# Optimization experiments

Measured on AMD Instinct MI355X. Metric: run time of the kernel, lower is better.

## Reference

```python
import jax, jax.numpy as jnp
import numpy as np

K = 8          # opt.pk, explicit precision cutoff
MARGIN = 0.2   # opt.margin
NEG = -1e30    # sentinel for masked sort keys


def setup_inputs() -> dict:
    key = jax.random.key(0)
    k1, k2 = jax.random.split(key)
    batch_reprs = jax.random.normal(k1, (4096, 512), dtype=jnp.float32)
    batch_labels = jax.random.randint(k2, (4096,), 0, 64)
    return {"batch_reprs": batch_reprs, "batch_labels": batch_labels}


def _forward(batch_reprs, batch_labels):
    B = batch_reprs.shape[0]
    dt = batch_reprs.dtype
    # cls_match_mat: 1 if same class
    match = (batch_labels[:, None] == batch_labels[None, :]).astype(dt)
    # pairwise euclidean distance (squared=False), safe sqrt at zero diagonal
    sq = jnp.sum(batch_reprs * batch_reprs, axis=1)
    res = jnp.maximum(sq[:, None] - 2.0 * (batch_reprs @ batch_reprs.T) + sq[None, :], 0.0)
    zero = res <= 0.0
    d = jnp.where(zero, 0.0, jnp.sqrt(jnp.where(zero, 1.0, res)))
    sim_hat = -d + (1.0 - match) * MARGIN  # use_margin=True path
    # rank via double argsort (descending similarity -> rank 1 = best)
    order = jnp.argsort(-sim_hat, axis=1)
    rank = jnp.argsort(order, axis=1).astype(dt) + 1.0
    pos_nums = jnp.sum(match, axis=1)
    ks = jnp.minimum(pos_nums, jnp.asarray(K + 1, dt))[:, None]  # k_mat per row
    w = 1.0 / jnp.log2(rank + 1.0) + 1.0  # DCG-style rank weight
    # false positives: not same class, within top-k_i
    fp_mask = (match < 1.0) & (rank <= ks)
    fp_nums = jnp.sum(fp_mask, axis=1)  # |N| per row
    # false negatives: same class, beyond top-k_i
    fn_mask = (match > 0.0) & (rank > ks)
    fp_term = jnp.sum(jnp.where(fp_mask, sim_hat * w, 0.0))
    # per-row variable-size topk over false negatives, vectorized:
    # mask non-FN entries to -inf, sort desc, keep first fp_nums[i] entries
    fn_key = jnp.where(fn_mask, sim_hat, NEG)
    fn_order = jnp.argsort(-fn_key, axis=1)
    sorted_sim = jnp.take_along_axis(sim_hat, fn_order, axis=1)
    sorted_w = jnp.take_along_axis(w, fn_order, axis=1)
    sorted_valid = jnp.take_along_axis(fn_mask, fn_order, axis=1)
    take = (jnp.arange(B)[None, :].astype(dt) < fp_nums[:, None]) & sorted_valid
    fn_term = jnp.sum(jnp.where(take, sorted_sim * sorted_w, 0.0))
    # rows with fp_num==0 contribute 0 to both terms, matching the host loop
    return fp_term - fn_term


def reference(batch_reprs, batch_labels):
    return _forward(batch_reprs, batch_labels)
```

## Files before the change

kernel.cpp:

```cpp
#include <hip/hip_runtime.h>
#include <math.h>

#define BB 4096
#define DD 512
#define KTOP 9
#define MARGIN_F 0.2f
#define NT 32
#define NTRI (NT * (NT + 1) / 2)

typedef __attribute__((ext_vector_type(8))) short short8;
typedef __attribute__((ext_vector_type(4))) float f32x4;
typedef unsigned long long u64;

__device__ unsigned short g_Rhi[(size_t)BB * DD];
__device__ u64 g_cmask[64 * 64];

__device__ __forceinline__ unsigned short f2bf(float x) {
  unsigned u = __float_as_uint(x);
  u += 0x7fffu + ((u >> 16) & 1u);
  return (unsigned short)(u >> 16);
}

__device__ __forceinline__ float ord16val(unsigned o16) {
  unsigned e = (o16 << 16) | 0x8000u;
  unsigned s = (e & 0x80000000u) ? (e ^ 0x80000000u) : ~e;
  return __uint_as_float(s);
}

__device__ __forceinline__ unsigned wavemax32_dpp(unsigned c) {
#define MSTEP(CTRL, RM)                                                        \
  {                                                                            \
    unsigned o = (unsigned)__builtin_amdgcn_update_dpp(0, (int)c, CTRL, RM, 0xf, false); \
    if (o > c) c = o;                                                          \
  }
  MSTEP(0xB1, 0xf) MSTEP(0x4E, 0xf) MSTEP(0x141, 0xf) MSTEP(0x140, 0xf)
  MSTEP(0x142, 0xa) MSTEP(0x143, 0xc)
#undef MSTEP
  return (unsigned)__builtin_amdgcn_readlane((int)c, 63);
}

__device__ __forceinline__ int wavesum_dpp(int c) {
#define SSTEP(CTRL, RM)                                                        \
  c += __builtin_amdgcn_update_dpp(0, c, CTRL, RM, 0xf, false);
  SSTEP(0xB1, 0xf) SSTEP(0x4E, 0xf) SSTEP(0x141, 0xf) SSTEP(0x140, 0xf)
  SSTEP(0x142, 0xa) SSTEP(0x143, 0xc)
#undef SSTEP
  return __builtin_amdgcn_readlane(c, 63);
}

__device__ __forceinline__ unsigned u4c(const uint4& f, int q) {
  return q == 0 ? f.x : q == 1 ? f.y : q == 2 ? f.z : f.w;
}

__global__ __launch_bounds__(64) void splitsq(const float* __restrict__ R,
                                              float* __restrict__ sq) {
  const int row = blockIdx.x, lane = threadIdx.x;
  const float4* r4 = (const float4*)(R + (size_t)row * DD);
  float4 a = r4[lane], b = r4[lane + 64];
  float xs[8] = {a.x, a.y, a.z, a.w, b.x, b.y, b.z, b.w};
  unsigned short hs[8];
  float s = 0.f;
  #pragma unroll
  for (int q = 0; q < 8; ++q) {
    float x = xs[q];
    s += x * x;
    hs[q] = f2bf(x);
  }
  const size_t base = (size_t)row * DD;
  *(ushort4*)&g_Rhi[base + lane * 4]       = *(ushort4*)&hs[0];
  *(ushort4*)&g_Rhi[base + 256 + lane * 4] = *(ushort4*)&hs[4];
  #pragma unroll
  for (int off = 32; off; off >>= 1) s += __shfl_down(s, off);
  if (lane == 0) sq[row] = s;
}

__global__ __launch_bounds__(64) void buildmask(const int* __restrict__ labels) {
  __shared__ int slab[BB];
  const int c = blockIdx.x, lane = threadIdx.x;
  for (int i = lane; i < BB / 4; i += 64) ((int4*)slab)[i] = ((const int4*)labels)[i];
  __syncthreads();
  u64 m = 0;
  #pragma unroll
  for (int e = 0; e < 64; ++e) {
    int j = 512 * (e >> 3) + 8 * lane + (e & 7);
    m |= (u64)(slab[j] == c) << e;
  }
  g_cmask[c * 64 + lane] = m;
}

__global__ __launch_bounds__(256, 2) void simgemm_rs2(const int* __restrict__ labels,
                                                      const float* __restrict__ sq,
                                                      unsigned short* __restrict__ simq) {
  const int x = blockIdx.x & 7;
  int c = blockIdx.x >> 3;
  int bi = 0, bj = 0;
  #pragma unroll
  for (int q = 0; q < 4; ++q) {
    const int bjq = (q < 2) ? (2 * x + q) : (28 - 2 * x + q);
    const int n = bjq + 1;
    if (c >= 0 && c < n) { bj = bjq; bi = c; }
    c -= n;
  }
  const int i0 = bi * 128, j0 = bj * 128;

  __shared__ __align__(16) unsigned char smembytes[65536];
  unsigned short (*kbuf)[2][8192] = (unsigned short (*)[2][8192])smembytes;

  const int tid = threadIdx.x;
  const int wid = tid >> 6, lane = tid & 63;
  const int wr = wid >> 1, wc = wid & 1;
  const int lrow = lane & 15, kblk = lane >> 4;

  const int sr = lane & 15;
  const int sc = (lane >> 4) * 8;
  const int r0 = (2 * wid + 0) * 16 + sr;
  const int r1 = (2 * wid + 1) * 16 + sr;
  const unsigned short* gA0 = &g_Rhi[(size_t)(i0 + r0) * DD + sc];
  const unsigned short* gA1 = &g_Rhi[(size_t)(i0 + r1) * DD + sc];
  const unsigned short* gB0 = &g_Rhi[(size_t)(j0 + r0) * DD + sc];
  const unsigned short* gB1 = &g_Rhi[(size_t)(j0 + r1) * DD + sc];

  f32x4 acc[4][4] = {};
  uint4 vA00, vA01, vA10, vA11, vB00, vB01, vB10, vB11;

#define STAGE_LOAD(K0)                                                         \
  vA00 = *(const uint4*)(gA0 + (K0));      vB00 = *(const uint4*)(gB0 + (K0)); \
  vA01 = *(const uint4*)(gA0 + (K0) + 32); vB01 = *(const uint4*)(gB0 + (K0) + 32); \
  vA10 = *(const uint4*)(gA1 + (K0));      vB10 = *(const uint4*)(gB1 + (K0)); \
  vA11 = *(const uint4*)(gA1 + (K0) + 32); vB11 = *(const uint4*)(gB1 + (K0) + 32);

#define STAGE_WRITE(BUF)                                                       \
  {                                                                            \
    const int c0 = (2 * wid + 0) * 1024 + lane * 8;                            \
    const int c1 = (2 * wid + 1) * 1024 + lane * 8;                            \
    *(uint4*)&kbuf[BUF][0][c0]       = vA00; *(uint4*)&kbuf[BUF][1][c0]       = vB00; \
    *(uint4*)&kbuf[BUF][0][c0 + 512] = vA01; *(uint4*)&kbuf[BUF][1][c0 + 512] = vB01; \
    *(uint4*)&kbuf[BUF][0][c1]       = vA10; *(uint4*)&kbuf[BUF][1][c1]       = vB10; \
    *(uint4*)&kbuf[BUF][0][c1 + 512] = vA11; *(uint4*)&kbuf[BUF][1][c1 + 512] = vB11; \
  }

  STAGE_LOAD(0);
  STAGE_WRITE(0);
  STAGE_LOAD(64);
  __syncthreads();

  for (int step = 0; step < 8; ++step) {
    const int cur = step & 1;

    #pragma unroll
    for (int kk = 0; kk < 2; ++kk) {
      short8 a[4], b[4];
      #pragma unroll
      for (int m = 0; m < 4; ++m)
        a[m] = *(const short8*)&kbuf[cur][0][(wr * 4 + m) * 1024 + kk * 512 + lane * 8];
      #pragma unroll
      for (int n = 0; n < 4; ++n)
        b[n] = *(const short8*)&kbuf[cur][1][(wc * 4 + n) * 1024 + kk * 512 + lane * 8];
      #pragma unroll
      for (int m = 0; m < 4; ++m) {
        #pragma unroll
        for (int n = 0; n < 4; ++n) {
          acc[m][n] = __builtin_amdgcn_mfma_f32_16x16x32_bf16(a[m], b[n], acc[m][n], 0, 0, 0);
        }
      }
    }

    if (step < 7) {
      STAGE_WRITE(cur ^ 1);
      if (step < 6) { STAGE_LOAD((step + 2) * 64); }
      __syncthreads();
    }
  }
#undef STAGE_LOAD
#undef STAGE_WRITE

  __syncthreads();
  unsigned short (*T)[132] = (unsigned short (*)[132])smembytes;
  float* sqi = (float*)(smembytes + 33792);
  float* sqj = (float*)(smembytes + 34304);
  int* labi  = (int*)(smembytes + 34816);
  int* labj  = (int*)(smembytes + 35328);
  if (tid < 128) { sqi[tid] = sq[i0 + tid]; labi[tid] = labels[i0 + tid]; }
  else { int t2 = tid - 128; sqj[t2] = sq[j0 + t2]; labj[t2] = labels[j0 + t2]; }
  __syncthreads();

  #pragma unroll
  for (int m = 0; m < 4; ++m) {
    const int rbase = wr * 64 + m * 16 + kblk * 4;
    #pragma unroll
    for (int n = 0; n < 4; ++n) {
      const int ccol = wc * 64 + n * 16 + lrow;
      const float sqc = sqj[ccol];
      const int lc_ = labj[ccol];
      #pragma unroll
      for (int reg = 0; reg < 4; ++reg) {
        const int r = rbase + reg;
        float res = sqi[r] - 2.0f * acc[m][n][reg] + sqc;
        float dd = (res <= 0.f) ? 0.f : sqrtf(res);
        float sv = -dd + ((labi[r] != lc_) ? MARGIN_F : 0.f);
        unsigned su = __float_as_uint(sv);
        unsigned ord = su ^ ((unsigned)((int)su >> 31) | 0x80000000u);
        T[r][ccol] = (unsigned short)(ord >> 16);
      }
    }
  }
  __syncthreads();

  const int srow0 = tid >> 4, scol0 = (tid & 15) * 8;
  #pragma unroll
  for (int p = 0; p < 8; ++p) {
    const int r = p * 16 + srow0;
    short8 w = *(const short8*)&T[r][scol0];
    *(short8*)&simq[(size_t)(i0 + r) * BB + j0 + scol0] = w;
  }
  if (bi != bj) {
    #pragma unroll
    for (int p = 0; p < 8; ++p) {
      const int col = p * 16 + srow0;
      unsigned short tmp[8];
      #pragma unroll
      for (int t = 0; t < 8; ++t) tmp[t] = T[scol0 + t][col];
      *(short8*)&simq[(size_t)(j0 + col) * BB + i0 + scol0] = *(short8*)tmp;
    }
  }
}

#define TOP2UPD(k, a, b) {                                                     \
  unsigned _mx = ((k) > (a)) ? (k) : (a);                                      \
  unsigned _mn = ((k) > (a)) ? (a) : (k);                                      \
  (a) = _mx;                                                                   \
  (b) = (_mn > (b)) ? _mn : (b); }

__global__ __launch_bounds__(256) void rowproc7(const unsigned short* __restrict__ simq,
                                                const int* __restrict__ labels,
                                                float* __restrict__ partials) {
  const int tid = threadIdx.x;
  const int lane = tid & 63;
  const int row = blockIdx.x * 4 + (tid >> 6);

  const int myl = labels[row];
  const u64 mask = g_cmask[myl * 64 + lane];
  const unsigned lbase2 = (unsigned)((4095 - 8 * lane) << 1);

  const uint4* rowp = (const uint4*)(simq + (size_t)row * BB);
  unsigned k[64];
  #pragma unroll
  for (int s = 0; s < 8; ++s) {
    uint4 w = rowp[lane + s * 64];
    const unsigned base_s = lbase2 - (unsigned)(1024 * s);
    #pragma unroll
    for (int q = 0; q < 4; ++q) {
      const unsigned wv = u4c(w, q);
      const int e0 = s * 8 + q * 2;
      k[e0]     = ((wv & 0xffffu) << 13)
                | (base_s - (unsigned)((q * 2) << 1)     + (unsigned)((mask >> e0) & 1ull));
      k[e0 + 1] = ((wv >> 16) << 13)
                | (base_s - (unsigned)((q * 2 + 1) << 1) + (unsigned)((mask >> (e0 + 1)) & 1ull));
    }
  }

  unsigned h1 = 0, h2 = 0;
  #pragma unroll
  for (int e = 0; e < 64; ++e) TOP2UPD(k[e], h1, h2);
  const int pos = wavesum_dpp(__popcll(mask));
  const int ks = min(pos, KTOP);

  unsigned kth = 0;
  float fp = 0.f; int fpn = 0;
  #pragma unroll
  for (int t = 0; t < KTOP; ++t) {
    if (t < ks) {
      unsigned g = wavemax32_dpp(h1);
      if (!(g & 1u)) { fp += ord16val(g >> 13) * (1.f / log2f((float)(t + 2)) + 1.f); fpn++; }
      if (t == ks - 1) kth = g;
      if (h1 == g) {
        h1 = h2; h2 = ~0u;
        if (h1 == ~0u) {
          h1 = 0; h2 = 0;
          #pragma unroll
          for (int e = 0; e < 64; ++e) {
            if (k[e] < g) TOP2UPD(k[e], h1, h2);
          }
        }
      }
    }
  }

  float fn = 0.f;
  if (fpn > 0) {
    unsigned f1 = 0, f2 = 0;
    #pragma unroll
    for (int e = 0; e < 64; ++e) {
      if ((k[e] & 1u) && k[e] < kth) TOP2UPD(k[e], f1, f2);
    }
    unsigned ck[KTOP];
    int nc = 0;
    #pragma unroll
    for (int u = 0; u < KTOP; ++u) {
      ck[u] = ~0u;
      if (u < fpn) {
        unsigned g = wavemax32_dpp(f1);
        if (g != 0u) {
          ck[u] = g; nc = u + 1;
          if (f1 == g) {
            f1 = f2; f2 = ~0u;
            if (f1 == ~0u) {
              f1 = 0; f2 = 0;
              #pragma unroll
              for (int e = 0; e < 64; ++e) {
                if ((k[e] & 1u) && k[e] < g) TOP2UPD(k[e], f1, f2);
              }
            }
          }
        }
      }
    }
    if (nc > 0) {
      int cnt[KTOP];
      #pragma unroll
      for (int u = 0; u < KTOP; ++u) cnt[u] = 0;
      #pragma unroll
      for (int e = 0; e < 64; ++e) {
        #pragma unroll
        for (int u = 0; u < KTOP; ++u) cnt[u] += (k[e] > ck[u]) ? 1 : 0;
      }
      #pragma unroll
      for (int u = 0; u < KTOP; ++u) cnt[u] = wavesum_dpp(cnt[u]);
      #pragma unroll
      for (int u = 0; u < KTOP; ++u) {
        if (u < nc) {
          int rank = 1 + cnt[u];
          fn += ord16val(ck[u] >> 13) * (1.f / log2f((float)(rank + 1)) + 1.f);
        }
      }
    }
  }

  if (lane == 0) partials[row] = fp - fn;
}

__global__ __launch_bounds__(256) void finalreduce(const float* __restrict__ partials,
                                                   float* __restrict__ out) {
  __shared__ float s[256];
  const int tid = threadIdx.x;
  float acc = 0.f;
  for (int j = tid; j < BB; j += 256) acc += partials[j];
  s[tid] = acc; __syncthreads();
  #pragma unroll
  for (int st = 128; st; st >>= 1) { if (tid < st) s[tid] += s[tid + st]; __syncthreads(); }
  if (tid == 0) out[0] = s[0];
}

extern "C" void kernel_launch(void* const* d_in, const int* in_sizes, int n_in,
                              void* d_out, int out_size, void* d_ws, size_t ws_size,
                              hipStream_t stream) {
  const float* R      = (const float*)d_in[0];
  const int*   labels = (const int*)d_in[1];
  float* out = (float*)d_out;

  unsigned short* simq = (unsigned short*)d_ws;
  float* sq            = (float*)((char*)d_ws + (size_t)BB * BB * 2);
  float* partials      = sq + BB;

  splitsq<<<BB, 64, 0, stream>>>(R, sq);
  buildmask<<<64, 64, 0, stream>>>(labels);
  simgemm_rs2<<<NTRI, 256, 0, stream>>>(labels, sq, simq);
  rowproc7<<<BB / 4, 256, 0, stream>>>(simq, labels, partials);
  finalreduce<<<1, 256, 0, stream>>>(partials, out);
}
```

Before: 93.88 us.

## Process four rows per wave in rowproc with software-prefetched next-row loads

Each wave in the row-processing kernel now handles four consecutive rows instead of one. It prefetches the next row's packed similarity data and class mask into registers while running the top-k selection on the current row. The grid shrinks from 1024 to 256 blocks, with launch bounds set to one block per SM. This aims to hide global-load latency behind the DPP reductions, at the cost of higher register pressure and fewer waves to hide latency across the GPU.

```diff
diff --git a/kernel.cpp b/kernel.cpp
--- a/kernel.cpp
+++ b/kernel.cpp
@@ -46,10 +46,6 @@
   SSTEP(0x142, 0xa) SSTEP(0x143, 0xc)
 #undef SSTEP
   return __builtin_amdgcn_readlane(c, 63);
-}
-
-__device__ __forceinline__ unsigned u4c(const uint4& f, int q) {
-  return q == 0 ? f.x : q == 1 ? f.y : q == 2 ? f.z : f.w;
 }
 
 __global__ __launch_bounds__(64) void splitsq(const float* __restrict__ R,
@@ -231,112 +227,135 @@
   (a) = _mx;                                                                   \
   (b) = (_mn > (b)) ? _mn : (b); }
 
-__global__ __launch_bounds__(256) void rowproc7(const unsigned short* __restrict__ simq,
-                                                const int* __restrict__ labels,
-                                                float* __restrict__ partials) {
+#define KB(S, W)                                                               \
+  {                                                                            \
+    const unsigned base_s = lbase2 - (unsigned)(1024 * (S));                   \
+    k[(S)*8+0] = (((W).x & 0xffffu) << 13) | (base_s -  0u + (unsigned)((mask >> ((S)*8+0)) & 1ull)); \
+    k[(S)*8+1] = (((W).x >> 16)     << 13) | (base_s -  2u + (unsigned)((mask >> ((S)*8+1)) & 1ull)); \
+    k[(S)*8+2] = (((W).y & 0xffffu) << 13) | (base_s -  4u + (unsigned)((mask >> ((S)*8+2)) & 1ull)); \
+    k[(S)*8+3] = (((W).y >> 16)     << 13) | (base_s -  6u + (unsigned)((mask >> ((S)*8+3)) & 1ull)); \
+    k[(S)*8+4] = (((W).z & 0xffffu) << 13) | (base_s -  8u + (unsigned)((mask >> ((S)*8+4)) & 1ull)); \
+    k[(S)*8+5] = (((W).z >> 16)     << 13) | (base_s - 10u + (unsigned)((mask >> ((S)*8+5)) & 1ull)); \
+    k[(S)*8+6] = (((W).w & 0xffffu) << 13) | (base_s - 12u + (unsigned)((mask >> ((S)*8+6)) & 1ull)); \
+    k[(S)*8+7] = (((W).w >> 16)     << 13) | (base_s - 14u + (unsigned)((mask >> ((S)*8+7)) & 1ull)); \
+  }
+
+__global__ __launch_bounds__(256, 1) void rowproc8(const unsigned short* __restrict__ simq,
+                                                   const int* __restrict__ labels,
+                                                   float* __restrict__ partials) {
   const int tid = threadIdx.x;
   const int lane = tid & 63;
-  const int row = blockIdx.x * 4 + (tid >> 6);
-
-  const int myl = labels[row];
-  const u64 mask = g_cmask[myl * 64 + lane];
+  const int row0 = blockIdx.x * 16 + (tid >> 6) * 4;
   const unsigned lbase2 = (unsigned)((4095 - 8 * lane) << 1);
 
-  const uint4* rowp = (const uint4*)(simq + (size_t)row * BB);
-  unsigned k[64];
-  #pragma unroll
-  for (int s = 0; s < 8; ++s) {
-    uint4 w = rowp[lane + s * 64];
-    const unsigned base_s = lbase2 - (unsigned)(1024 * s);
-    #pragma unroll
-    for (int q = 0; q < 4; ++q) {
-      const unsigned wv = u4c(w, q);
-      const int e0 = s * 8 + q * 2;
-      k[e0]     = ((wv & 0xffffu) << 13)
-                | (base_s - (unsigned)((q * 2) << 1)     + (unsigned)((mask >> e0) & 1ull));
-      k[e0 + 1] = ((wv >> 16) << 13)
-                | (base_s - (unsigned)((q * 2 + 1) << 1) + (unsigned)((mask >> (e0 + 1)) & 1ull));
-    }
-  }
-
-  unsigned h1 = 0, h2 = 0;
-  #pragma unroll
-  for (int e = 0; e < 64; ++e) TOP2UPD(k[e], h1, h2);
-  const int pos = wavesum_dpp(__popcll(mask));
-  const int ks = min(pos, KTOP);
-
-  unsigned kth = 0;
-  float fp = 0.f; int fpn = 0;
-  #pragma unroll
-  for (int t = 0; t < KTOP; ++t) {
-    if (t < ks) {
-      unsigned g = wavemax32_dpp(h1);
-      if (!(g & 1u)) { fp += ord16val(g >> 13) * (1.f / log2f((float)(t + 2)) + 1.f); fpn++; }
-      if (t == ks - 1) kth = g;
-      if (h1 == g) {
-        h1 = h2; h2 = ~0u;
-        if (h1 == ~0u) {
-          h1 = 0; h2 = 0;
-          #pragma unroll
-          for (int e = 0; e < 64; ++e) {
-            if (k[e] < g) TOP2UPD(k[e], h1, h2);
+  uint4 w0, w1, w2, w3, w4, w5, w6, w7;
+  {
+    const uint4* rp = (const uint4*)(simq + (size_t)row0 * BB);
+    w0 = rp[lane];       w1 = rp[lane + 64];  w2 = rp[lane + 128]; w3 = rp[lane + 192];
+    w4 = rp[lane + 256]; w5 = rp[lane + 320]; w6 = rp[lane + 384]; w7 = rp[lane + 448];
+  }
+  int myl = labels[row0];
+  u64 mask = g_cmask[myl * 64 + lane];
+
+  for (int rr = 0; rr < 4; ++rr) {
+    const int row = row0 + rr;
+
+    unsigned k[64];
+    KB(0, w0) KB(1, w1) KB(2, w2) KB(3, w3)
+    KB(4, w4) KB(5, w5) KB(6, w6) KB(7, w7)
+    const int pos = wavesum_dpp(__popcll(mask));
+    const int ks = min(pos, KTOP);
+
+    int nlab = 0;
+    if (rr < 3) {
+      const uint4* rp = (const uint4*)(simq + (size_t)(row + 1) * BB);
+      w0 = rp[lane];       w1 = rp[lane + 64];  w2 = rp[lane + 128]; w3 = rp[lane + 192];
+      w4 = rp[lane + 256]; w5 = rp[lane + 320]; w6 = rp[lane + 384]; w7 = rp[lane + 448];
+      nlab = labels[row + 1];
+    }
+
+    unsigned h1 = 0, h2 = 0;
+    #pragma unroll
+    for (int e = 0; e < 64; ++e) TOP2UPD(k[e], h1, h2);
+
+    unsigned kth = 0;
+    float fp = 0.f; int fpn = 0;
+    #pragma unroll
+    for (int t = 0; t < KTOP; ++t) {
+      if (t < ks) {
+        unsigned g = wavemax32_dpp(h1);
+        if (!(g & 1u)) { fp += ord16val(g >> 13) * (1.f / log2f((float)(t + 2)) + 1.f); fpn++; }
+        if (t == ks - 1) kth = g;
+        if (h1 == g) {
+          h1 = h2; h2 = ~0u;
+          if (h1 == ~0u) {
+            h1 = 0; h2 = 0;
+            #pragma unroll
+            for (int e = 0; e < 64; ++e) {
+              if (k[e] < g) TOP2UPD(k[e], h1, h2);
+            }
           }
         }
       }
     }
-  }
-
-  float fn = 0.f;
-  if (fpn > 0) {
-    unsigned f1 = 0, f2 = 0;
-    #pragma unroll
-    for (int e = 0; e < 64; ++e) {
-      if ((k[e] & 1u) && k[e] < kth) TOP2UPD(k[e], f1, f2);
-    }
-    unsigned ck[KTOP];
-    int nc = 0;
-    #pragma unroll
-    for (int u = 0; u < KTOP; ++u) {
-      ck[u] = ~0u;
-      if (u < fpn) {
-        unsigned g = wavemax32_dpp(f1);
-        if (g != 0u) {
-          ck[u] = g; nc = u + 1;
-          if (f1 == g) {
-            f1 = f2; f2 = ~0u;
-            if (f1 == ~0u) {
-              f1 = 0; f2 = 0;
-              #pragma unroll
-              for (int e = 0; e < 64; ++e) {
-                if ((k[e] & 1u) && k[e] < g) TOP2UPD(k[e], f1, f2);
+
+    u64 nmask = 0;
+    if (rr < 3) nmask = g_cmask[nlab * 64 + lane];
+
+    float fn = 0.f;
+    if (fpn > 0) {
+      unsigned f1 = 0, f2 = 0;
+      #pragma unroll
+      for (int e = 0; e < 64; ++e) {
+        if ((k[e] & 1u) && k[e] < kth) TOP2UPD(k[e], f1, f2);
+      }
+      unsigned ck[KTOP];
+      int nc = 0;
+      #pragma unroll
+      for (int u = 0; u < KTOP; ++u) {
+        ck[u] = ~0u;
+        if (u < fpn) {
+          unsigned g = wavemax32_dpp(f1);
+          if (g != 0u) {
+            ck[u] = g; nc = u + 1;
+            if (f1 == g) {
+              f1 = f2; f2 = ~0u;
+              if (f1 == ~0u) {
+                f1 = 0; f2 = 0;
+                #pragma unroll
+                for (int e = 0; e < 64; ++e) {
+                  if ((k[e] & 1u) && k[e] < g) TOP2UPD(k[e], f1, f2);
+                }
               }
             }
           }
         }
       }
-    }
-    if (nc > 0) {
-      int cnt[KTOP];
-      #pragma unroll
-      for (int u = 0; u < KTOP; ++u) cnt[u] = 0;
-      #pragma unroll
-      for (int e = 0; e < 64; ++e) {
-        #pragma unroll
-        for (int u = 0; u < KTOP; ++u) cnt[u] += (k[e] > ck[u]) ? 1 : 0;
-      }
-      #pragma unroll
-      for (int u = 0; u < KTOP; ++u) cnt[u] = wavesum_dpp(cnt[u]);
-      #pragma unroll
-      for (int u = 0; u < KTOP; ++u) {
-        if (u < nc) {
-          int rank = 1 + cnt[u];
-          fn += ord16val(ck[u] >> 13) * (1.f / log2f((float)(rank + 1)) + 1.f);
-        }
-      }
-    }
-  }
-
-  if (lane == 0) partials[row] = fp - fn;
+      if (nc > 0) {
+        int cnt[KTOP];
+        #pragma unroll
+        for (int u = 0; u < KTOP; ++u) cnt[u] = 0;
+        #pragma unroll
+        for (int e = 0; e < 64; ++e) {
+          #pragma unroll
+          for (int u = 0; u < KTOP; ++u) cnt[u] += (k[e] > ck[u]) ? 1 : 0;
+        }
+        #pragma unroll
+        for (int u = 0; u < KTOP; ++u) cnt[u] = wavesum_dpp(cnt[u]);
+        #pragma unroll
+        for (int u = 0; u < KTOP; ++u) {
+          if (u < nc) {
+            int rank = 1 + cnt[u];
+            fn += ord16val(ck[u] >> 13) * (1.f / log2f((float)(rank + 1)) + 1.f);
+          }
+        }
+      }
+    }
+
+    if (lane == 0) partials[row] = fp - fn;
+    myl = nlab;
+    mask = nmask;
+  }
 }
 
 __global__ __launch_bounds__(256) void finalreduce(const float* __restrict__ partials,
@@ -365,6 +384,6 @@
   splitsq<<<BB, 64, 0, stream>>>(R, sq);
   buildmask<<<64, 64, 0, stream>>>(labels);
   simgemm_rs2<<<NTRI, 256, 0, stream>>>(labels, sq, simq);
-  rowproc7<<<BB / 4, 256, 0, stream>>>(simq, labels, partials);
+  rowproc8<<<256, 256, 0, stream>>>(simq, labels, partials);
   finalreduce<<<1, 256, 0, stream>>>(partials, out);
 }
```

After: 118.0 us. +25.7%, slower.

## Split each row's top-k selection across two waves with shared-memory merges

Applied to the files above, without the earlier changes.

Row processing now runs one row per 128-thread block, and each of its two wavefronts holds half of the row's 4096 keys (32 per lane instead of 64). Wave-level max and count results are merged through shared memory with block barriers. The aim is to halve per-lane register pressure and serial scan length, raising occupancy and latency hiding. The cost is extra __syncthreads per selection step and twice as many waves per row.

```diff
diff --git a/kernel.cpp b/kernel.cpp
--- a/kernel.cpp
+++ b/kernel.cpp
@@ -231,46 +231,65 @@
   (a) = _mx;                                                                   \
   (b) = (_mn > (b)) ? _mn : (b); }
 
-__global__ __launch_bounds__(256) void rowproc7(const unsigned short* __restrict__ simq,
+__global__ __launch_bounds__(128) void rowproc9(const unsigned short* __restrict__ simq,
                                                 const int* __restrict__ labels,
                                                 float* __restrict__ partials) {
+  __shared__ unsigned sred[2 * KTOP + 2][2];
+  __shared__ int sint[2 + 2 * KTOP];
+
   const int tid = threadIdx.x;
   const int lane = tid & 63;
-  const int row = blockIdx.x * 4 + (tid >> 6);
+  const int h = tid >> 6;
+  const int row = blockIdx.x;
+
+  const uint4* rp = (const uint4*)(simq + (size_t)row * BB);
+  uint4 w0 = rp[lane + (4 * h + 0) * 64];
+  uint4 w1 = rp[lane + (4 * h + 1) * 64];
+  uint4 w2 = rp[lane + (4 * h + 2) * 64];
+  uint4 w3 = rp[lane + (4 * h + 3) * 64];
 
   const int myl = labels[row];
-  const u64 mask = g_cmask[myl * 64 + lane];
+  const unsigned mh = (unsigned)(g_cmask[myl * 64 + lane] >> (32 * h));
   const unsigned lbase2 = (unsigned)((4095 - 8 * lane) << 1);
 
-  const uint4* rowp = (const uint4*)(simq + (size_t)row * BB);
-  unsigned k[64];
-  #pragma unroll
-  for (int s = 0; s < 8; ++s) {
-    uint4 w = rowp[lane + s * 64];
-    const unsigned base_s = lbase2 - (unsigned)(1024 * s);
+  unsigned k[32];
+  #pragma unroll
+  for (int s = 0; s < 4; ++s) {
+    const uint4 w = s == 0 ? w0 : s == 1 ? w1 : s == 2 ? w2 : w3;
+    const unsigned base_s = lbase2 - (unsigned)(1024 * (4 * h + s));
     #pragma unroll
     for (int q = 0; q < 4; ++q) {
       const unsigned wv = u4c(w, q);
       const int e0 = s * 8 + q * 2;
       k[e0]     = ((wv & 0xffffu) << 13)
-                | (base_s - (unsigned)((q * 2) << 1)     + (unsigned)((mask >> e0) & 1ull));
+                | (base_s - (unsigned)((q * 2) << 1)     + ((mh >> e0) & 1u));
       k[e0 + 1] = ((wv >> 16) << 13)
-                | (base_s - (unsigned)((q * 2 + 1) << 1) + (unsigned)((mask >> (e0 + 1)) & 1ull));
-    }
-  }
+                | (base_s - (unsigned)((q * 2 + 1) << 1) + ((mh >> (e0 + 1)) & 1u));
+    }
+  }
+
+  {
+    int p = wavesum_dpp(__popc(mh));
+    sint[h] = p;
+  }
+  __syncthreads();
+  const int pos = sint[0] + sint[1];
+  const int ks = min(pos, KTOP);
 
   unsigned h1 = 0, h2 = 0;
   #pragma unroll
-  for (int e = 0; e < 64; ++e) TOP2UPD(k[e], h1, h2);
-  const int pos = wavesum_dpp(__popcll(mask));
-  const int ks = min(pos, KTOP);
+  for (int e = 0; e < 32; ++e) TOP2UPD(k[e], h1, h2);
 
   unsigned kth = 0;
   float fp = 0.f; int fpn = 0;
   #pragma unroll
   for (int t = 0; t < KTOP; ++t) {
     if (t < ks) {
-      unsigned g = wavemax32_dpp(h1);
+      sred[t][h] = wavemax32_dpp(h1);
+    }
+    __syncthreads();
+    if (t < ks) {
+      const unsigned g = max(sred[t][0], sred[t][1]);
       if (!(g & 1u)) { fp += ord16val(g >> 13) * (1.f / log2f((float)(t + 2)) + 1.f); fpn++; }
       if (t == ks - 1) kth = g;
       if (h1 == g) {
@@ -278,7 +297,7 @@
         if (h1 == ~0u) {
           h1 = 0; h2 = 0;
           #pragma unroll
-          for (int e = 0; e < 64; ++e) {
+          for (int e = 0; e < 32; ++e) {
             if (k[e] < g) TOP2UPD(k[e], h1, h2);
           }
         }
@@ -290,7 +309,7 @@
   if (fpn > 0) {
     unsigned f1 = 0, f2 = 0;
     #pragma unroll
-    for (int e = 0; e < 64; ++e) {
+    for (int e = 0; e < 32; ++e) {
       if ((k[e] & 1u) && k[e] < kth) TOP2UPD(k[e], f1, f2);
     }
     unsigned ck[KTOP];
@@ -299,7 +318,11 @@
     for (int u = 0; u < KTOP; ++u) {
       ck[u] = ~0u;
       if (u < fpn) {
-        unsigned g = wavemax32_dpp(f1);
+        sred[KTOP + 1 + u][h] = wavemax32_dpp(f1);
+      }
+      __syncthreads();
+      if (u < fpn) {
+        const unsigned g = max(sred[KTOP + 1 + u][0], sred[KTOP + 1 + u][1]);
         if (g != 0u) {
           ck[u] = g; nc = u + 1;
           if (f1 == g) {
@@ -307,7 +330,7 @@
             if (f1 == ~0u) {
               f1 = 0; f2 = 0;
               #pragma unroll
-              for (int e = 0; e < 64; ++e) {
+              for (int e = 0; e < 32; ++e) {
                 if ((k[e] & 1u) && k[e] < g) TOP2UPD(k[e], f1, f2);
               }
             }
@@ -320,23 +343,28 @@
       #pragma unroll
       for (int u = 0; u < KTOP; ++u) cnt[u] = 0;
       #pragma unroll
-      for (int e = 0; e < 64; ++e) {
+      for (int e = 0; e < 32; ++e) {
         #pragma unroll
         for (int u = 0; u < KTOP; ++u) cnt[u] += (k[e] > ck[u]) ? 1 : 0;
       }
       #pragma unroll
-      for (int u = 0; u < KTOP; ++u) cnt[u] = wavesum_dpp(cnt[u]);
+      for (int u = 0; u < KTOP; ++u) {
+        sint[2 + h * KTOP + u] = wavesum_dpp(cnt[u]);
+      }
+    }
+    __syncthreads();
+    if (nc > 0) {
       #pragma unroll
       for (int u = 0; u < KTOP; ++u) {
         if (u < nc) {
-          int rank = 1 + cnt[u];
+          const int rank = 1 + sint[2 + u] + sint[2 + KTOP + u];
           fn += ord16val(ck[u] >> 13) * (1.f / log2f((float)(rank + 1)) + 1.f);
         }
       }
     }
   }
 
-  if (lane == 0) partials[row] = fp - fn;
+  if (tid == 0) partials[row] = fp - fn;
 }
 
 __global__ __launch_bounds__(256) void finalreduce(const float* __restrict__ partials,
@@ -365,6 +393,6 @@
   splitsq<<<BB, 64, 0, stream>>>(R, sq);
   buildmask<<<64, 64, 0, stream>>>(labels);
   simgemm_rs2<<<NTRI, 256, 0, stream>>>(labels, sq, simq);
-  rowproc7<<<BB / 4, 256, 0, stream>>>(simq, labels, partials);
+  rowproc9<<<BB, 128, 0, stream>>>(simq, labels, partials);
   finalreduce<<<1, 256, 0, stream>>>(partials, out);
 }
```

New measurement: 93.06 us. Within noise of the previous version (-0.9%).
